# Performance work log

Hardware: AMD Instinct MI355X
Metric: run time of the kernel (lower is better)

The kernel has to match this reference:

```python
import jax, jax.numpy as jnp
import numpy as np
import math

H = 1024
N = 64  # state size; N2 = N // 2 complex modes
DT_MIN, DT_MAX = 0.001, 0.1


def setup_inputs() -> dict:
    key = jax.random.key(0)
    k1, k2 = jax.random.split(key)
    N2 = N // 2
    # C is declared zeros in the buggy source; use randn so the output is non-trivial
    C = jax.random.normal(k1, (H, N2), dtype=jnp.float32)
    log_dt = math.log(DT_MIN) + jax.random.uniform(k2, (H,), dtype=jnp.float32) * (
        math.log(DT_MAX) - math.log(DT_MIN)
    )
    log_A_real = jnp.full((H, N2), math.log(0.5), dtype=jnp.float32)
    A_imag = math.pi * jnp.broadcast_to(jnp.arange(N2, dtype=jnp.float32), (H, N2))
    return {
        "C": C,
        "log_dt": log_dt,
        "log_A_real": log_A_real,
        "A_imag": A_imag,
        "L": 4096,
    }


def reference(C, log_dt, log_A_real, A_imag, L):
    dt = jnp.exp(log_dt)  # (H,)
    A = -jnp.exp(log_A_real) + 1j * A_imag  # (H, N2) complex
    dtA = A * dt[:, None].astype(A.dtype)  # (H, N2)
    # Vandermonde: exp(dtA[h,n] * l) for l in [0, L)  -> (H, N2, L)
    P = jnp.exp(dtA[:, :, None] * jnp.arange(L, dtype=jnp.float32))
    Cc = C.astype(dtA.dtype) * (jnp.exp(dtA) - 1.0) / A  # (H, N2)
    K = 2.0 * jnp.einsum("hn,hnl->hl", Cc, P)  # (H, L) complex
    return K.real
```

## Files before the change

### kernel.cpp

```cpp
#include <hip/hip_runtime.h>


static __device__ __forceinline__ float2 cmul(float2 a, float2 b) {
    return make_float2(fmaf(a.x, b.x, -(a.y * b.y)),
                       fmaf(a.x, b.y,   a.y * b.x));
}

template <int N2, int BLK, int J>
__global__ __launch_bounds__(BLK, 4) void s4d_kernel(
    const float* __restrict__ C,
    const float* __restrict__ log_dt,
    const float* __restrict__ log_A_real,
    const float* __restrict__ A_imag,
    float* __restrict__ K,
    int L)
{
    __shared__ float4 s_lop[N2][16];
    __shared__ float4 s_hip[N2][16];

    const int h = blockIdx.x;
    const int y = blockIdx.y;
    const int lbase = y * (BLK * J);
    const int t = threadIdx.x;

    {
        const int n  = t >> 3;
        const int e  = t & 7;
        const int kk = e * 2;

        const float dt  = expf(log_dt[h]);
        const float Are = -expf(log_A_real[h * N2 + n]);
        const float Aim = A_imag[h * N2 + n];
        const float dre = Are * dt;
        const float dim = Aim * dt;
        float sw, cw;
        sincosf(dim, &sw, &cw);
        const float er = expf(dre);
        const float2 w = make_float2(er * cw, er * sw);
        const float nre = w.x - 1.0f;
        const float nim = w.y;
        const float inv = 1.0f / (Are * Are + Aim * Aim);
        const float2 c  = make_float2(
            2.0f * C[h * N2 + n] * ((nre * Are + nim * Aim) * inv),
            2.0f * C[h * N2 + n] * ((nim * Are - nre * Aim) * inv));
        const float2 w2   = cmul(w,    w);
        const float2 w4   = cmul(w2,   w2);
        const float2 w8   = cmul(w4,   w4);
        const float2 w16  = cmul(w8,   w8);
        const float2 w32  = cmul(w16,  w16);
        const float2 w64  = cmul(w32,  w32);
        const float2 w128 = cmul(w64,  w64);
        const float2 W    = cmul(w128, w128);
        const float aW = W.x + W.x;
        const float bW = -fmaf(W.x, W.x, W.y * W.y);

        const float2 ONE = make_float2(1.0f, 0.0f);
        const float2 f1 = (e & 1) ? w2 : ONE;
        const float2 f2 = (e & 2) ? w4 : ONE;
        const float2 f3 = (e & 4) ? w8 : ONE;
        const float2 pk = cmul(cmul(f1, f2), f3);
        const float2 g1 = (e & 1) ? w32  : ONE;
        const float2 g2 = (e & 2) ? w64  : ONE;
        const float2 g3 = (e & 4) ? w128 : ONE;
        const float2 qk = cmul(cmul(g1, g2), g3);

        float2 P = ONE;
        {
            float2 base = W;
            int ee = J * y;
            while (ee) { if (ee & 1) P = cmul(P, base); base = cmul(base, base); ee >>= 1; }
        }

        const float2 lo0  = cmul(cmul(c, P), pk);
        const float2 lo1  = cmul(lo0, w);
        const float2 lo20 = cmul(lo0, W);
        const float2 lo21 = cmul(lo1, W);
        s_lop[n][kk]     = make_float4(lo0.x, lo0.y, lo20.x, lo20.y);
        s_lop[n][kk + 1] = make_float4(lo1.x, lo1.y, lo21.x, lo21.y);

        const float2 hi1 = cmul(qk, w16);
        s_hip[n][kk]     = make_float4(qk.x,  qk.y,  aW, bW);
        s_hip[n][kk + 1] = make_float4(hi1.x, hi1.y, aW, bW);
    }
    __syncthreads();

    float acc[J];
#pragma unroll
    for (int j = 0; j < J; ++j) acc[j] = 0.0f;

    const int tlo = t & 15;
    const int thi = t >> 4;

#pragma unroll 2
    for (int n = 0; n < N2; ++n) {
        const float4 lp = s_lop[n][tlo];
        const float4 hp = s_hip[n][thi];

        float x0 = fmaf(lp.x, hp.x, -(lp.y * hp.y));
        float x1 = fmaf(lp.z, hp.x, -(lp.w * hp.y));
        acc[0] += x0;
        acc[1] += x1;
#pragma unroll
        for (int j = 2; j < J; ++j) {
            const float x2 = fmaf(hp.z, x1, hp.w * x0);
            acc[j] += x2;
            x0 = x1;
            x1 = x2;
        }
    }

    float* __restrict__ outp = K + (size_t)h * (size_t)L + lbase + t;
#pragma unroll
    for (int j = 0; j < J; ++j) {
        const int l = lbase + j * BLK + t;
        if (l < L) outp[(size_t)j * BLK] = acc[j];
    }
}

extern "C" void kernel_launch(void* const* d_in, const int* in_sizes, int n_in,
                              void* d_out, int out_size, void* d_ws, size_t ws_size,
                              hipStream_t stream)
{
    const float* C          = (const float*)d_in[0];
    const float* log_dt     = (const float*)d_in[1];
    const float* log_A_real = (const float*)d_in[2];
    const float* A_imag     = (const float*)d_in[3];
    float* K = (float*)d_out;

    const int H   = in_sizes[1];
    const int N2v = in_sizes[0] / H;
    const int L   = out_size / H;
    constexpr int BLK = 256;
    constexpr int J   = 16;
    const int gy = (L + BLK * J - 1) / (BLK * J);

    if (N2v != 32) return;
    dim3 grid((unsigned)H, (unsigned)gy);
    s4d_kernel<32, BLK, J><<<grid, BLK, 0, stream>>>(
        C, log_dt, log_A_real, A_imag, K, L);
}
```

Before: 78.20 us.

## Split mode sum across two thread groups with shared-memory reduction

Doubles the block to 512 threads and splits the 32 complex modes into two halves, each half handled by its own group of 256 threads over the same output columns. The partial sums are then combined through shared memory before the store. The setup phase now gives one thread per (mode, k) table entry instead of two entries per thread. The aim is more parallelism and latency hiding per output tile, at the cost of an extra barrier, a shared-memory reduction, and more threads in the prologue.

Result: no change. 78.46 us (+0.3%).

```diff
diff --git a/kernel.cpp b/kernel.cpp
--- a/kernel.cpp
+++ b/kernel.cpp
@@ -6,8 +6,8 @@
                        fmaf(a.x, b.y,   a.y * b.x));
 }
 
-template <int N2, int BLK, int J>
-__global__ __launch_bounds__(BLK, 4) void s4d_kernel(
+template <int N2, int CPB, int J>
+__global__ __launch_bounds__(2 * CPB, 8) void s4d_kernel(
     const float* __restrict__ C,
     const float* __restrict__ log_dt,
     const float* __restrict__ log_A_real,
@@ -15,18 +15,19 @@
     float* __restrict__ K,
     int L)
 {
+    constexpr int MPG = N2 / 2;
     __shared__ float4 s_lop[N2][16];
     __shared__ float4 s_hip[N2][16];
+    __shared__ float4 s_part[J / 4][CPB];
 
     const int h = blockIdx.x;
     const int y = blockIdx.y;
-    const int lbase = y * (BLK * J);
+    const int lbase = y * (CPB * J);
     const int t = threadIdx.x;
 
     {
-        const int n  = t >> 3;
-        const int e  = t & 7;
-        const int kk = e * 2;
+        const int n = t >> 4;
+        const int k = t & 15;
 
         const float dt  = expf(log_dt[h]);
         const float Are = -expf(log_A_real[h * N2 + n]);
@@ -40,9 +41,9 @@
         const float nre = w.x - 1.0f;
         const float nim = w.y;
         const float inv = 1.0f / (Are * Are + Aim * Aim);
-        const float2 c  = make_float2(
-            2.0f * C[h * N2 + n] * ((nre * Are + nim * Aim) * inv),
-            2.0f * C[h * N2 + n] * ((nim * Are - nre * Aim) * inv));
+        const float cc  = 2.0f * C[h * N2 + n];
+        const float2 c  = make_float2(cc * ((nre * Are + nim * Aim) * inv),
+                                      cc * ((nim * Are - nre * Aim) * inv));
         const float2 w2   = cmul(w,    w);
         const float2 w4   = cmul(w2,   w2);
         const float2 w8   = cmul(w4,   w4);
@@ -55,14 +56,14 @@
         const float bW = -fmaf(W.x, W.x, W.y * W.y);
 
         const float2 ONE = make_float2(1.0f, 0.0f);
-        const float2 f1 = (e & 1) ? w2 : ONE;
-        const float2 f2 = (e & 2) ? w4 : ONE;
-        const float2 f3 = (e & 4) ? w8 : ONE;
-        const float2 pk = cmul(cmul(f1, f2), f3);
-        const float2 g1 = (e & 1) ? w32  : ONE;
-        const float2 g2 = (e & 2) ? w64  : ONE;
-        const float2 g3 = (e & 4) ? w128 : ONE;
-        const float2 qk = cmul(cmul(g1, g2), g3);
+        float2 pk = (k & 1) ? w : ONE;
+        pk = cmul(pk, (k & 2) ? w2 : ONE);
+        pk = cmul(pk, (k & 4) ? w4 : ONE);
+        pk = cmul(pk, (k & 8) ? w8 : ONE);
+        float2 qk = (k & 1) ? w16 : ONE;
+        qk = cmul(qk, (k & 2) ? w32  : ONE);
+        qk = cmul(qk, (k & 4) ? w64  : ONE);
+        qk = cmul(qk, (k & 8) ? w128 : ONE);
 
         float2 P = ONE;
         {
@@ -71,16 +72,10 @@
             while (ee) { if (ee & 1) P = cmul(P, base); base = cmul(base, base); ee >>= 1; }
         }
 
-        const float2 lo0  = cmul(cmul(c, P), pk);
-        const float2 lo1  = cmul(lo0, w);
-        const float2 lo20 = cmul(lo0, W);
-        const float2 lo21 = cmul(lo1, W);
-        s_lop[n][kk]     = make_float4(lo0.x, lo0.y, lo20.x, lo20.y);
-        s_lop[n][kk + 1] = make_float4(lo1.x, lo1.y, lo21.x, lo21.y);
-
-        const float2 hi1 = cmul(qk, w16);
-        s_hip[n][kk]     = make_float4(qk.x,  qk.y,  aW, bW);
-        s_hip[n][kk + 1] = make_float4(hi1.x, hi1.y, aW, bW);
+        const float2 lo  = cmul(cmul(c, P), pk);
+        const float2 lo2 = cmul(lo, W);
+        s_lop[n][k] = make_float4(lo.x, lo.y, lo2.x, lo2.y);
+        s_hip[n][k] = make_float4(qk.x, qk.y, aW, bW);
     }
     __syncthreads();
 
@@ -88,13 +83,16 @@
 #pragma unroll
     for (int j = 0; j < J; ++j) acc[j] = 0.0f;
 
-    const int tlo = t & 15;
-    const int thi = t >> 4;
+    const int col = t & (CPB - 1);
+    const int g   = t / CPB;
+    const int tlo = col & 15;
+    const int thi = col >> 4;
+    const int nb  = g * MPG;
 
 #pragma unroll 2
-    for (int n = 0; n < N2; ++n) {
-        const float4 lp = s_lop[n][tlo];
-        const float4 hp = s_hip[n][thi];
+    for (int nn = 0; nn < MPG; ++nn) {
+        const float4 lp = s_lop[nb + nn][tlo];
+        const float4 hp = s_hip[nb + nn][thi];
 
         float x0 = fmaf(lp.x, hp.x, -(lp.y * hp.y));
         float x1 = fmaf(lp.z, hp.x, -(lp.w * hp.y));
@@ -109,11 +107,27 @@
         }
     }
 
-    float* __restrict__ outp = K + (size_t)h * (size_t)L + lbase + t;
+    if (g == 1) {
 #pragma unroll
-    for (int j = 0; j < J; ++j) {
-        const int l = lbase + j * BLK + t;
-        if (l < L) outp[(size_t)j * BLK] = acc[j];
+        for (int q = 0; q < J / 4; ++q)
+            s_part[q][col] = make_float4(acc[4*q], acc[4*q+1], acc[4*q+2], acc[4*q+3]);
+    }
+    __syncthreads();
+    if (g == 0) {
+        float* __restrict__ outp = K + (size_t)h * (size_t)L + lbase + col;
+#pragma unroll
+        for (int q = 0; q < J / 4; ++q) {
+            const float4 p = s_part[q][col];
+            const float r0 = acc[4*q]     + p.x;
+            const float r1 = acc[4*q + 1] + p.y;
+            const float r2 = acc[4*q + 2] + p.z;
+            const float r3 = acc[4*q + 3] + p.w;
+            const int l0 = lbase + (4*q) * CPB + col;
+            if (l0 < L)             outp[(size_t)(4*q)     * CPB] = r0;
+            if (l0 + CPB < L)       outp[(size_t)(4*q + 1) * CPB] = r1;
+            if (l0 + 2 * CPB < L)   outp[(size_t)(4*q + 2) * CPB] = r2;
+            if (l0 + 3 * CPB < L)   outp[(size_t)(4*q + 3) * CPB] = r3;
+        }
     }
 }
 
@@ -130,12 +144,12 @@
     const int H   = in_sizes[1];
     const int N2v = in_sizes[0] / H;
     const int L   = out_size / H;
-    constexpr int BLK = 256;
+    constexpr int CPB = 256;
     constexpr int J   = 16;
-    const int gy = (L + BLK * J - 1) / (BLK * J);
+    const int gy = (L + CPB * J - 1) / (CPB * J);
 
     if (N2v != 32) return;
     dim3 grid((unsigned)H, (unsigned)gy);
-    s4d_kernel<32, BLK, J><<<grid, BLK, 0, stream>>>(
+    s4d_kernel<32, CPB, J><<<grid, 2 * CPB, 0, stream>>>(
         C, log_dt, log_A_real, A_imag, K, L);
 }
```
